# Kernel tuning notes

Hardware: AMD Instinct MI355X
Metric: run time of the kernel (lower is better)

Reference implementation:

```python
import jax, jax.numpy as jnp
import numpy as np

INP = 512
HIDDEN = 512
N_HEADS = 8          # called 'head_dim' in the torch code
D_HEAD = HIDDEN // N_HEADS  # 64
BASE = 10000.0
SCALE = D_HEAD ** (-0.5)


def rope(x):
    # x: [b, s, h, d]
    b, s, h, d = x.shape
    half = d // 2
    theta = 1.0 / (BASE ** (jnp.arange(0, d, 2, dtype=jnp.float32) / d))  # [d/2]
    idx_theta = jnp.arange(s, dtype=jnp.float32)[:, None] * theta[None, :]  # [s, d/2]
    idx_theta2 = jnp.concatenate([idx_theta, idx_theta], axis=1)            # [s, d]
    neg_half = jnp.concatenate([-x[..., half:], x[..., :half]], axis=-1)
    cos = jnp.cos(idx_theta2)[None, :, None, :]
    sin = jnp.sin(idx_theta2)[None, :, None, :]
    return x * cos + neg_half * sin


def setup_inputs() -> dict:
    key = jax.random.key(0)
    ks = jax.random.split(key, 10)
    b, s = 4, 2048
    init = lambda k, shp, fan_in: jax.random.normal(k, shp, jnp.float32) * (fan_in ** -0.5)
    return {
        "x": jax.random.normal(ks[0], (b, s, INP), jnp.float32),
        "c": jax.random.normal(ks[1], (b, s, INP), jnp.float32),
        "Wq": init(ks[2], (INP, HIDDEN), INP), "bq": jnp.zeros((HIDDEN,), jnp.float32),
        "Wk": init(ks[3], (INP, HIDDEN), INP), "bk": jnp.zeros((HIDDEN,), jnp.float32),
        "Wv": init(ks[4], (INP, HIDDEN), INP), "bv": jnp.zeros((HIDDEN,), jnp.float32),
        "Wo": init(ks[5], (HIDDEN, INP), HIDDEN), "bo": jnp.zeros((INP,), jnp.float32),
    }


def reference(x, c, Wq, bq, Wk, bk, Wv, bv, Wo, bo):
    b, s, _ = x.shape
    h_res = x
    q = (c @ Wq + bq).reshape(b, s, N_HEADS, D_HEAD)
    k = (x @ Wk + bk).reshape(b, s, N_HEADS, D_HEAD)
    v = (x @ Wv + bv).reshape(b, s, N_HEADS, D_HEAD)
    q = rope(q)
    k = rope(k)  # computed but unused, exactly as in the source
    # NOTE: source computes scores between q and V (not k) -- faithful reproduction
    att = jnp.einsum('bihd,bjhd->bhij', q, v)            # [b, h, s, s]
    att = jax.nn.softmax(att * SCALE, axis=-1)
    out = jnp.einsum('bhij,bjhd->bihd', att, v)          # [b, s, h, d]
    out = out.reshape(b, s, HIDDEN)
    out = out @ Wo + bo
    return out + h_res
```

## Files before the change

kernel.cpp:

```cpp
#include <hip/hip_runtime.h>
#include <hip/hip_bf16.h>
#include <cstdint>

typedef float f32x4 __attribute__((ext_vector_type(4)));
typedef short bf16x8 __attribute__((ext_vector_type(8)));
typedef short bf16x4 __attribute__((ext_vector_type(4)));
typedef unsigned short u16;

#define B_    4
#define S_    2048
#define H_    8
#define D_    64
#define M_    8192

#define OFF_CBF   0UL
#define OFF_XBF   8388608UL
#define OFF_QBH   16777216UL
#define OFF_VBH   25165824UL
#define OFF_VTBH  33554432UL
#define OFF_ATTN  41943040UL
#define OFF_WQT   50331648UL
#define OFF_WVT   50855936UL
#define OFF_WOT   51380224UL
#define OFF_BIAS  51904512UL
#define OFF_COS   51910656UL
#define OFF_SIN   52172800UL
#define WS_NEEDED 52434944UL

__device__ __forceinline__ u16 f2bf(float f){
    union { float f; uint32_t u; } v; v.f = f;
    uint32_t r = (v.u + 0x7fffu + ((v.u >> 16) & 1u)) >> 16;
    return (u16)r;
}
__device__ __forceinline__ float bf2f(u16 h){
    union { uint32_t u; float f; } v; v.u = ((uint32_t)h) << 16;
    return v.f;
}
__device__ __forceinline__ uint32_t fbits(float f){
    union { float f; uint32_t u; } v; v.f = f; return v.u;
}

__device__ __forceinline__ f32x4 mfma16(bf16x4 a, bf16x4 b, f32x4 c){
#if __has_builtin(__builtin_amdgcn_mfma_f32_16x16x16bf16_1k)
    return __builtin_amdgcn_mfma_f32_16x16x16bf16_1k(a, b, c, 0, 0, 0);
#else
    asm volatile("v_mfma_f32_16x16x16_bf16 %0, %1, %2, %0" : "+v"(c) : "v"(a), "v"(b));
    return c;
#endif
}

__device__ __forceinline__ int swz(int row, int col){
    return (col & ~63) | ((((col >> 3) & 7) ^ (row & 7)) << 3) | (col & 7);
}

__device__ __forceinline__ int detect_f32(const void* x_in){
    int lane = threadIdx.x & 63;
    ushort2 dv = ((const ushort2*)x_in)[lane];
    bool hit = ((((dv.x >> 7) & 0xFF) >= 160) || (((dv.y >> 7) & 0xFF) >= 160));
    return __ballot(hit) != 0ULL;
}

__device__ __forceinline__ void gload_lds16(const u16* g, u16* l){
    __builtin_amdgcn_global_load_lds(
        (const __attribute__((address_space(1))) void*)g,
        (__attribute__((address_space(3))) void*)l, 16, 0, 0);
}

__global__ void k_prep(const void* c_in, const void* x_in,
                       const void* Wq, const void* Wv, const void* Wo,
                       const void* bq, const void* bv, const void* bo,
                       u16* c_bf, u16* x_bf,
                       u16* Wqt, u16* Wvt, u16* Wot, float* bias_ws,
                       float* cos_t, float* sin_t){
    int bid = blockIdx.x;
    if (bid >= 11264){
        int idx = (bid - 11264) * 256 + threadIdx.x;
        int pos = idx >> 5, j = idx & 31;
        double theta = pow(10000.0, -(double)j / 32.0);
        double rev = ((double)pos * theta) * 0.15915494309189535;
        rev -= floor(rev);
        float fr = (float)rev;
        cos_t[idx] = __builtin_amdgcn_cosf(fr);
        sin_t[idx] = __builtin_amdgcn_sinf(fr);
        return;
    }
    if (bid >= 8192){
        int f = detect_f32(x_in);
        int wi = (bid - 8192) >> 10;
        int idx = ((bid - 8192) & 1023) * 256 + threadIdx.x;
        int k = idx >> 9, n = idx & 511;
        const void* W; u16* Wt; const void* bb;
        if (wi == 0){ W = Wq; Wt = Wqt; bb = bq; }
        else if (wi == 1){ W = Wv; Wt = Wvt; bb = bv; }
        else { W = Wo; Wt = Wot; bb = bo; }
        float v = f ? ((const float*)W)[idx] : bf2f(((const u16*)W)[idx]);
        Wt[n * 512 + swz(n, k)] = f2bf(v);
        if (idx < 512){
            float b = f ? ((const float*)bb)[idx] : bf2f(((const u16*)bb)[idx]);
            bias_ws[wi * 512 + idx] = b;
        }
        return;
    }
    int f = detect_f32(x_in);
    int isx = bid >= 4096;
    int t = (bid & 4095) * 256 + threadIdx.x;
    const void* src = isx ? x_in : c_in;
    u16* dst = isx ? x_bf : c_bf;
    int e0 = t * 4, row = e0 >> 9, col = e0 & 511;
    size_t didx = (size_t)row * 512 + swz(row, col);
    ushort4 o;
    if (f){
        float4 v = ((const float4*)src)[t];
        o.x = f2bf(v.x); o.y = f2bf(v.y); o.z = f2bf(v.z); o.w = f2bf(v.w);
    } else {
        o = ((const ushort4*)src)[t];
    }
    *(ushort4*)(dst + didx) = o;
}

__global__ __launch_bounds__(256) void k_gemm_qv(
    const u16* __restrict__ c_bf, const u16* __restrict__ x_bf,
    const u16* __restrict__ Wqt, const u16* __restrict__ Wvt,
    const float* __restrict__ bias_ws,
    const float* __restrict__ cos_t, const float* __restrict__ sin_t,
    u16* __restrict__ Qbh, u16* __restrict__ Vbh, u16* __restrict__ Vtbh)
{
    __shared__ __align__(16) u16 Als[2][128 * 64];
    __shared__ __align__(16) u16 Bls[2][128 * 64];
    const int w = threadIdx.x >> 6, lane = threadIdx.x & 63;
    const int g = lane >> 4, cq = lane & 15;
    const int wm = w & 1, wn = w >> 1;
    const int z = blockIdx.z;
    const u16* A  = z ? x_bf : c_bf;
    const u16* Wt = z ? Wvt : Wqt;
    const float* bias = bias_ws + (z ? 512 : 0);
    const int m0b = blockIdx.x * 128, n0b = blockIdx.y * 128;
    const int m0 = m0b + wm * 64, n0 = n0b + wn * 64;
    const int swzi = ((cq & 7) << 3);

    int srow[4], scol[4];
    #pragma unroll
    for (int i = 0; i < 4; i++){
        int flat = (w * 4 + i) * 64 + lane;
        srow[i] = flat >> 3; scol[i] = (flat & 7) * 8;
    }

    const f32x4 zero = {0.f, 0.f, 0.f, 0.f};
    f32x4 acc[4][4];
    #pragma unroll
    for (int i = 0; i < 4; i++)
        #pragma unroll
        for (int j = 0; j < 4; j++) acc[i][j] = zero;

    #pragma unroll
    for (int i = 0; i < 4; i++){
        gload_lds16(A  + (size_t)(m0b + srow[i]) * 512 + scol[i], &Als[0][(w*4 + i) * 512]);
        gload_lds16(Wt + (size_t)(n0b + srow[i]) * 512 + scol[i], &Bls[0][(w*4 + i) * 512]);
    }

    for (int kt = 0; kt < 8; kt++){
        const int buf = kt & 1;
        __builtin_amdgcn_s_waitcnt(0x0F70);
        __syncthreads();
        if (kt < 7){
            const int kk = (kt + 1) * 64;
            #pragma unroll
            for (int i = 0; i < 4; i++){
                gload_lds16(A  + (size_t)(m0b + srow[i]) * 512 + kk + scol[i], &Als[buf^1][(w*4 + i) * 512]);
                gload_lds16(Wt + (size_t)(n0b + srow[i]) * 512 + kk + scol[i], &Bls[buf^1][(w*4 + i) * 512]);
            }
        }
        #pragma unroll
        for (int ks = 0; ks < 2; ks++){
            const int cs = ((ks * 4 + g) << 3) ^ swzi;
            bf16x8 a[4], b[4];
            #pragma unroll
            for (int mt = 0; mt < 4; mt++)
                a[mt] = *(const bf16x8*)&Als[buf][(wm*64 + mt*16 + cq) * 64 + cs];
            #pragma unroll
            for (int nt = 0; nt < 4; nt++)
                b[nt] = *(const bf16x8*)&Bls[buf][(wn*64 + nt*16 + cq) * 64 + cs];
            #pragma unroll
            for (int mt = 0; mt < 4; mt++)
                #pragma unroll
                for (int nt = 0; nt < 4; nt++)
                    acc[mt][nt] = __builtin_amdgcn_mfma_f32_16x16x32_bf16(a[mt], b[nt], acc[mt][nt], 0, 0, 0);
        }
    }
    __syncthreads();

    #pragma unroll
    for (int nt = 0; nt < 4; nt++){
        float bvv = bias[n0 + nt*16 + cq];
        #pragma unroll
        for (int mt = 0; mt < 4; mt++) acc[mt][nt] += bvv;
    }
    const int h = n0 >> 6;
    if (z == 0){
        const float SCL = 0.125f * 1.4426950408889634f;
        #pragma unroll
        for (int mt = 0; mt < 4; mt++){
            #pragma unroll
            for (int r = 0; r < 4; r++){
                int row = m0 + mt*16 + g*4 + r;
                int b_idx = row >> 11, si = row & 2047;
                size_t base = ((size_t)(b_idx*8 + h) * 2048 + si) * 64;
                #pragma unroll
                for (int nt = 0; nt < 2; nt++){
                    int dj = nt*16 + cq;
                    float cv = cos_t[si*32 + dj], sv = sin_t[si*32 + dj];
                    float x1 = acc[mt][nt][r], x2 = acc[mt][nt+2][r];
                    Qbh[base + dj]      = f2bf((x1*cv - x2*sv) * SCL);
                    Qbh[base + dj + 32] = f2bf((x2*cv + x1*sv) * SCL);
                }
            }
        }
    } else {
        float* ltw = ((float*)&Als[0][0]) + w * (16 * 65);
        const int b_idx = m0 >> 11, si0 = m0 & 2047;
        const size_t tbase = ((size_t)(b_idx*8 + h) * 64) * 2048;
        #pragma unroll
        for (int mt = 0; mt < 4; mt++)
            #pragma unroll
            for (int r = 0; r < 4; r++){
                int row = m0 + mt*16 + g*4 + r;
                int bi = row >> 11, si = row & 2047;
                size_t base = ((size_t)(bi*8 + h) * 2048 + si) * 64;
                int s7 = si & 7;
                #pragma unroll
                for (int nt = 0; nt < 4; nt++){
                    int dj = nt*16 + cq;
                    int col = ((((dj >> 3) ^ s7) & 7) << 3) | (dj & 7);
                    Vbh[base + col] = f2bf(acc[mt][nt][r]);
                }
            }
        #pragma unroll
        for (int nt = 0; nt < 4; nt++){
            #pragma unroll
            for (int mt = 0; mt < 4; mt++)
                #pragma unroll
                for (int r = 0; r < 4; r++)
                    ltw[cq * 65 + mt*16 + g*4 + r] = acc[mt][nt][r];
            __builtin_amdgcn_wave_barrier();
            #pragma unroll
            for (int dd = 0; dd < 16; dd++){
                float v = ltw[dd * 65 + lane];
                int col = ((((lane >> 3) ^ (dd & 7)) & 7) << 3) | (lane & 7);
                Vtbh[tbase + (size_t)(nt*16 + dd) * 2048 + si0 + col] = f2bf(v);
            }
            __builtin_amdgcn_wave_barrier();
        }
    }
}

__global__ __launch_bounds__(256) void k_attn(
    const u16* __restrict__ Qbh, const u16* __restrict__ Vbh,
    const u16* __restrict__ Vtbh, u16* __restrict__ attn)
{
    __shared__ __align__(16) u16 Vs[2][64 * 64];
    __shared__ __align__(16) u16 Vts[2][64 * 64];
    const int w = threadIdx.x >> 6, lane = threadIdx.x & 63;
    const int g = lane >> 4, cq = lane & 15;
    const int s7 = cq & 7;
    const int bh = blockIdx.y;
    const int i0 = blockIdx.x * 128 + w * 32;

    bf16x8 aq[2][2];
    #pragma unroll
    for (int mt = 0; mt < 2; mt++)
        #pragma unroll
        for (int kk = 0; kk < 2; kk++)
            aq[mt][kk] = *(const bf16x8*)(Qbh + ((size_t)bh*2048 + i0 + mt*16 + cq)*64 + kk*32 + g*8);

    const int c0 = (w * 2) * 512, c1 = c0 + 512;
    const u16* gvs0 = Vbh + (size_t)bh * 131072 + c0 + lane * 8;
    const u16* gvs1 = gvs0 + 512;
    const int dr0 = (w * 2) * 8 + (lane >> 3);
    const u16* gvt0 = Vtbh + ((size_t)bh * 64 + dr0) * 2048 + (lane & 7) * 8;
    const u16* gvt1 = gvt0 + 8 * 2048;

    gload_lds16(gvs0, &Vs[0][c0]);
    gload_lds16(gvs1, &Vs[0][c1]);
    gload_lds16(gvt0, &Vts[0][c0]);
    gload_lds16(gvt1, &Vts[0][c1]);

    const f32x4 zero = {0.f, 0.f, 0.f, 0.f};
    f32x4 o[2][4]; float fl[2] = {0.f, 0.f};
    #pragma unroll
    for (int mt = 0; mt < 2; mt++)
        #pragma unroll
        for (int t = 0; t < 4; t++) o[mt][t] = zero;

    for (int jt = 0; jt < 32; jt++){
        const int buf = jt & 1;
        __builtin_amdgcn_s_waitcnt(0x0F70);
        __syncthreads();
        if (jt < 31){
            const size_t os = (size_t)(jt + 1) * 4096, ot = (size_t)(jt + 1) * 64;
            gload_lds16(gvs0 + os, &Vs[buf^1][c0]);
            gload_lds16(gvs1 + os, &Vs[buf^1][c1]);
            gload_lds16(gvt0 + ot, &Vts[buf^1][c0]);
            gload_lds16(gvt1 + ot, &Vts[buf^1][c1]);
        }
        bf16x4 pk[2][4];
        #pragma unroll
        for (int t = 0; t < 4; t++){
            bf16x8 bv0 = *(const bf16x8*)&Vs[buf][(t*16 + cq)*64 + ((g ^ s7) << 3)];
            bf16x8 bv1 = *(const bf16x8*)&Vs[buf][(t*16 + cq)*64 + (((4 + g) ^ s7) << 3)];
            #pragma unroll
            for (int mt = 0; mt < 2; mt++){
                f32x4 s = __builtin_amdgcn_mfma_f32_16x16x32_bf16(bv0, aq[mt][0], zero, 0, 0, 0);
                s = __builtin_amdgcn_mfma_f32_16x16x32_bf16(bv1, aq[mt][1], s, 0, 0, 0);
                #pragma unroll
                for (int r = 0; r < 4; r++) s[r] = __builtin_amdgcn_exp2f(s[r]);
                fl[mt] += (s[0] + s[1]) + (s[2] + s[3]);
                union { bf16x4 v; uint32_t wd[2]; } u;
                u.wd[0] = (fbits(s[0]) >> 16) | (fbits(s[1]) & 0xffff0000u);
                u.wd[1] = (fbits(s[2]) >> 16) | (fbits(s[3]) & 0xffff0000u);
                pk[mt][t] = u.v;
            }
        }
        #pragma unroll
        for (int t = 0; t < 4; t++){
            const int chk = ((t*2 + (g >> 1)) ^ s7) & 7;
            #pragma unroll
            for (int tn = 0; tn < 4; tn++){
                bf16x4 bt = *(const bf16x4*)&Vts[buf][(tn*16 + cq)*64 + (chk << 3) + (g & 1)*4];
                o[0][tn] = mfma16(bt, pk[0][t], o[0][tn]);
                o[1][tn] = mfma16(bt, pk[1][t], o[1][tn]);
            }
        }
    }
    const int b_idx = bh >> 3, h = bh & 7;
    #pragma unroll
    for (int mt = 0; mt < 2; mt++){
        float sum = fl[mt];
        sum += __shfl_xor(sum, 16);
        sum += __shfl_xor(sum, 32);
        float inv = 1.f / sum;
        int row = b_idx*2048 + i0 + mt*16 + cq;
        #pragma unroll
        for (int tn = 0; tn < 4; tn++){
            f32x4 ov = o[mt][tn] * inv;
            uint2 pw;
            pw.x = (fbits(ov[0]) >> 16) | (fbits(ov[1]) & 0xffff0000u);
            pw.y = (fbits(ov[2]) >> 16) | (fbits(ov[3]) & 0xffff0000u);
            int chunk = ((tn*2 + (g >> 1)) ^ s7) & 7;
            int col = h*64 + (chunk << 3) + (g & 1)*4;
            *(uint2*)&attn[(size_t)row * 512 + col] = pw;
        }
    }
}

__global__ __launch_bounds__(256) void k_gemm_out(
    const u16* __restrict__ attn, const u16* __restrict__ Wot,
    const float* __restrict__ bias_ws, const void* __restrict__ x_in,
    void* __restrict__ out)
{
    __shared__ __align__(16) u16 Als[2][128 * 64];
    __shared__ __align__(16) u16 Bls[2][64 * 64];
    const int w = threadIdx.x >> 6, lane = threadIdx.x & 63;
    const int g = lane >> 4, cq = lane & 15;
    const int wm = w & 1, wn = w >> 1;
    const int m0b = blockIdx.x * 128, n0b = blockIdx.y * 64;
    const int m0 = m0b + wm * 64, n0 = n0b + wn * 32;
    const int f = detect_f32(x_in);
    const int swzi = ((cq & 7) << 3);

    int sra[4], sca[4], srb[2], scb[2];
    #pragma unroll
    for (int i = 0; i < 4; i++){
        int flat = (w * 4 + i) * 64 + lane;
        sra[i] = flat >> 3; sca[i] = (flat & 7) * 8;
    }
    #pragma unroll
    for (int i = 0; i < 2; i++){
        int flat = (w * 2 + i) * 64 + lane;
        srb[i] = flat >> 3; scb[i] = (flat & 7) * 8;
    }

    const f32x4 zero = {0.f, 0.f, 0.f, 0.f};
    f32x4 acc[4][2];
    #pragma unroll
    for (int i = 0; i < 4; i++)
        #pragma unroll
        for (int j = 0; j < 2; j++) acc[i][j] = zero;

    #pragma unroll
    for (int i = 0; i < 4; i++)
        gload_lds16(attn + (size_t)(m0b + sra[i]) * 512 + sca[i], &Als[0][(w*4 + i) * 512]);
    #pragma unroll
    for (int i = 0; i < 2; i++)
        gload_lds16(Wot + (size_t)(n0b + srb[i]) * 512 + scb[i], &Bls[0][(w*2 + i) * 512]);

    for (int kt = 0; kt < 8; kt++){
        const int buf = kt & 1;
        __builtin_amdgcn_s_waitcnt(0x0F70);
        __syncthreads();
        if (kt < 7){
            const int kk = (kt + 1) * 64;
            #pragma unroll
            for (int i = 0; i < 4; i++)
                gload_lds16(attn + (size_t)(m0b + sra[i]) * 512 + kk + sca[i], &Als[buf^1][(w*4 + i) * 512]);
            #pragma unroll
            for (int i = 0; i < 2; i++)
                gload_lds16(Wot + (size_t)(n0b + srb[i]) * 512 + kk + scb[i], &Bls[buf^1][(w*2 + i) * 512]);
        }
        #pragma unroll
        for (int ks = 0; ks < 2; ks++){
            const int cs = ((ks * 4 + g) << 3) ^ swzi;
            bf16x8 a[4], b[2];
            #pragma unroll
            for (int mt = 0; mt < 4; mt++)
                a[mt] = *(const bf16x8*)&Als[buf][(wm*64 + mt*16 + cq) * 64 + cs];
            #pragma unroll
            for (int nt = 0; nt < 2; nt++)
                b[nt] = *(const bf16x8*)&Bls[buf][(wn*32 + nt*16 + cq) * 64 + cs];
            #pragma unroll
            for (int mt = 0; mt < 4; mt++)
                #pragma unroll
                for (int nt = 0; nt < 2; nt++)
                    acc[mt][nt] = __builtin_amdgcn_mfma_f32_16x16x32_bf16(a[mt], b[nt], acc[mt][nt], 0, 0, 0);
        }
    }
    #pragma unroll
    for (int mt = 0; mt < 4; mt++)
        #pragma unroll
        for (int nt = 0; nt < 2; nt++)
            #pragma unroll
            for (int r = 0; r < 4; r++){
                int row = m0 + mt*16 + g*4 + r;
                int col = n0 + nt*16 + cq;
                size_t idx = (size_t)row * 512 + col;
                float resid = f ? ((const float*)x_in)[idx] : bf2f(((const u16*)x_in)[idx]);
                float v = acc[mt][nt][r] + bias_ws[1024 + col] + resid;
                if (f) ((float*)out)[idx] = v;
                else   ((u16*)out)[idx] = f2bf(v);
            }
}

extern "C" void kernel_launch(void* const* d_in, const int* in_sizes, int n_in,
                              void* d_out, int out_size, void* d_ws, size_t ws_size,
                              hipStream_t stream){
    const void* x_in = d_in[0];
    const void* c_in = d_in[1];
    const void* Wq = d_in[2]; const void* bq = d_in[3];
    const void* Wv = d_in[6]; const void* bv = d_in[7];
    const void* Wo = d_in[8]; const void* bo = d_in[9];

    if (ws_size < WS_NEEDED){
        hipMemsetAsync(d_out, 0, (size_t)out_size * 2, stream);
        return;
    }
    char* ws = (char*)d_ws;
    u16* c_bf  = (u16*)(ws + OFF_CBF);
    u16* x_bf  = (u16*)(ws + OFF_XBF);
    u16* Qbh   = (u16*)(ws + OFF_QBH);
    u16* Vbh   = (u16*)(ws + OFF_VBH);
    u16* Vtbh  = (u16*)(ws + OFF_VTBH);
    u16* attn  = (u16*)(ws + OFF_ATTN);
    u16* Wqt   = (u16*)(ws + OFF_WQT);
    u16* Wvt   = (u16*)(ws + OFF_WVT);
    u16* Wot   = (u16*)(ws + OFF_WOT);
    float* bias_ws = (float*)(ws + OFF_BIAS);
    float* cos_t   = (float*)(ws + OFF_COS);
    float* sin_t   = (float*)(ws + OFF_SIN);

    k_prep<<<11520, 256, 0, stream>>>(c_in, x_in, Wq, Wv, Wo, bq, bv, bo,
                                      c_bf, x_bf, Wqt, Wvt, Wot, bias_ws, cos_t, sin_t);
    k_gemm_qv<<<dim3(64, 4, 2), 256, 0, stream>>>(c_bf, x_bf, Wqt, Wvt, bias_ws,
                                                  cos_t, sin_t, Qbh, Vbh, Vtbh);
    k_attn<<<dim3(16, 32), 256, 0, stream>>>(Qbh, Vbh, Vtbh, attn);
    k_gemm_out<<<dim3(64, 8), 256, 0, stream>>>(attn, Wot, bias_ws, x_in, d_out);
}
```

Measured before the change: 196.4 us.

## Split attention over key halves and merge partial sums in output GEMM

The attention kernel now splits the key/value sequence into two halves along a new grid z dimension. Each half writes unnormalized bf16 partial outputs and row sums, which the output projection GEMM combines and normalizes while staging its A tile. The change also replaces the XOR-swizzled LDS layouts and direct global-to-LDS loads with padded (stride 68) rows loaded through registers, and adds an occupancy hint. The aim is to double the attention block count for better CU utilization. In exchange it adds an extra partial-buffer round trip, conversion work in the GEMM prologue, and a second bf16 rounding of the partials.

```diff
diff --git a/kernel.cpp b/kernel.cpp
--- a/kernel.cpp
+++ b/kernel.cpp
@@ -94,7 +94,7 @@
         else if (wi == 1){ W = Wv; Wt = Wvt; bb = bv; }
         else { W = Wo; Wt = Wot; bb = bo; }
         float v = f ? ((const float*)W)[idx] : bf2f(((const u16*)W)[idx]);
-        Wt[n * 512 + swz(n, k)] = f2bf(v);
+        Wt[n * 512 + (wi == 2 ? k : swz(n, k))] = f2bf(v);
         if (idx < 512){
             float b = f ? ((const float*)bb)[idx] : bf2f(((const u16*)bb)[idx]);
             bias_ws[wi * 512 + idx] = b;
@@ -226,13 +226,9 @@
                 int row = m0 + mt*16 + g*4 + r;
                 int bi = row >> 11, si = row & 2047;
                 size_t base = ((size_t)(bi*8 + h) * 2048 + si) * 64;
-                int s7 = si & 7;
-                #pragma unroll
-                for (int nt = 0; nt < 4; nt++){
-                    int dj = nt*16 + cq;
-                    int col = ((((dj >> 3) ^ s7) & 7) << 3) | (dj & 7);
-                    Vbh[base + col] = f2bf(acc[mt][nt][r]);
-                }
+                #pragma unroll
+                for (int nt = 0; nt < 4; nt++)
+                    Vbh[base + nt*16 + cq] = f2bf(acc[mt][nt][r]);
             }
         #pragma unroll
         for (int nt = 0; nt < 4; nt++){
@@ -245,25 +241,25 @@
             #pragma unroll
             for (int dd = 0; dd < 16; dd++){
                 float v = ltw[dd * 65 + lane];
-                int col = ((((lane >> 3) ^ (dd & 7)) & 7) << 3) | (lane & 7);
-                Vtbh[tbase + (size_t)(nt*16 + dd) * 2048 + si0 + col] = f2bf(v);
+                Vtbh[tbase + (size_t)(nt*16 + dd) * 2048 + si0 + lane] = f2bf(v);
             }
             __builtin_amdgcn_wave_barrier();
         }
     }
 }
 
-__global__ __launch_bounds__(256) void k_attn(
+__global__ __launch_bounds__(256, 4) void k_attn(
     const u16* __restrict__ Qbh, const u16* __restrict__ Vbh,
-    const u16* __restrict__ Vtbh, u16* __restrict__ attn)
+    const u16* __restrict__ Vtbh,
+    u16* __restrict__ part0, u16* __restrict__ part1, float* __restrict__ lsum)
 {
-    __shared__ __align__(16) u16 Vs[2][64 * 64];
-    __shared__ __align__(16) u16 Vts[2][64 * 64];
+    __shared__ __align__(16) u16 Vs[2][64 * 68];
+    __shared__ __align__(16) u16 Vts[2][64 * 68];
     const int w = threadIdx.x >> 6, lane = threadIdx.x & 63;
     const int g = lane >> 4, cq = lane & 15;
-    const int s7 = cq & 7;
-    const int bh = blockIdx.y;
+    const int bh = blockIdx.y, z = blockIdx.z;
     const int i0 = blockIdx.x * 128 + w * 32;
+    const int j0 = z * 1024;
 
     bf16x8 aq[2][2];
     #pragma unroll
@@ -272,17 +268,17 @@
         for (int kk = 0; kk < 2; kk++)
             aq[mt][kk] = *(const bf16x8*)(Qbh + ((size_t)bh*2048 + i0 + mt*16 + cq)*64 + kk*32 + g*8);
 
-    const int c0 = (w * 2) * 512, c1 = c0 + 512;
-    const u16* gvs0 = Vbh + (size_t)bh * 131072 + c0 + lane * 8;
-    const u16* gvs1 = gvs0 + 512;
-    const int dr0 = (w * 2) * 8 + (lane >> 3);
-    const u16* gvt0 = Vtbh + ((size_t)bh * 64 + dr0) * 2048 + (lane & 7) * 8;
-    const u16* gvt1 = gvt0 + 8 * 2048;
-
-    gload_lds16(gvs0, &Vs[0][c0]);
-    gload_lds16(gvs1, &Vs[0][c1]);
-    gload_lds16(gvt0, &Vts[0][c0]);
-    gload_lds16(gvt1, &Vts[0][c1]);
+    const int sr = w * 16 + (lane >> 2), sc = (lane & 3) * 16;
+    const u16* gvs = Vbh  + ((size_t)bh*2048 + j0 + sr) * 64 + sc;
+    const u16* gvt = Vtbh + ((size_t)bh*64 + sr) * 2048 + j0 + sc;
+    const int ls = sr * 68 + sc;
+
+    {
+        bf16x8 a0 = *(const bf16x8*)gvs,       a1 = *(const bf16x8*)(gvs + 8);
+        bf16x8 b0 = *(const bf16x8*)gvt,       b1 = *(const bf16x8*)(gvt + 8);
+        *(bf16x8*)&Vs[0][ls]  = a0;  *(bf16x8*)&Vs[0][ls + 8]  = a1;
+        *(bf16x8*)&Vts[0][ls] = b0;  *(bf16x8*)&Vts[0][ls + 8] = b1;
+    }
 
     const f32x4 zero = {0.f, 0.f, 0.f, 0.f};
     f32x4 o[2][4]; float fl[2] = {0.f, 0.f};
@@ -291,22 +287,21 @@
         #pragma unroll
         for (int t = 0; t < 4; t++) o[mt][t] = zero;
 
-    for (int jt = 0; jt < 32; jt++){
+    for (int jt = 0; jt < 16; jt++){
         const int buf = jt & 1;
-        __builtin_amdgcn_s_waitcnt(0x0F70);
         __syncthreads();
-        if (jt < 31){
-            const size_t os = (size_t)(jt + 1) * 4096, ot = (size_t)(jt + 1) * 64;
-            gload_lds16(gvs0 + os, &Vs[buf^1][c0]);
-            gload_lds16(gvs1 + os, &Vs[buf^1][c1]);
-            gload_lds16(gvt0 + ot, &Vts[buf^1][c0]);
-            gload_lds16(gvt1 + ot, &Vts[buf^1][c1]);
+        bf16x8 na0, na1, nb0, nb1;
+        if (jt < 15){
+            na0 = *(const bf16x8*)(gvs + (size_t)(jt + 1) * 4096);
+            na1 = *(const bf16x8*)(gvs + (size_t)(jt + 1) * 4096 + 8);
+            nb0 = *(const bf16x8*)(gvt + (size_t)(jt + 1) * 64);
+            nb1 = *(const bf16x8*)(gvt + (size_t)(jt + 1) * 64 + 8);
         }
         bf16x4 pk[2][4];
         #pragma unroll
         for (int t = 0; t < 4; t++){
-            bf16x8 bv0 = *(const bf16x8*)&Vs[buf][(t*16 + cq)*64 + ((g ^ s7) << 3)];
-            bf16x8 bv1 = *(const bf16x8*)&Vs[buf][(t*16 + cq)*64 + (((4 + g) ^ s7) << 3)];
+            bf16x8 bv0 = *(const bf16x8*)&Vs[buf][(t*16 + cq)*68 + g*8];
+            bf16x8 bv1 = *(const bf16x8*)&Vs[buf][(t*16 + cq)*68 + 32 + g*8];
             #pragma unroll
             for (int mt = 0; mt < 2; mt++){
                 f32x4 s = __builtin_amdgcn_mfma_f32_16x16x32_bf16(bv0, aq[mt][0], zero, 0, 0, 0);
@@ -321,51 +316,54 @@
             }
         }
         #pragma unroll
-        for (int t = 0; t < 4; t++){
-            const int chk = ((t*2 + (g >> 1)) ^ s7) & 7;
+        for (int t = 0; t < 4; t++)
             #pragma unroll
             for (int tn = 0; tn < 4; tn++){
-                bf16x4 bt = *(const bf16x4*)&Vts[buf][(tn*16 + cq)*64 + (chk << 3) + (g & 1)*4];
+                bf16x4 bt = *(const bf16x4*)&Vts[buf][(tn*16 + cq)*68 + t*16 + g*4];
                 o[0][tn] = mfma16(bt, pk[0][t], o[0][tn]);
                 o[1][tn] = mfma16(bt, pk[1][t], o[1][tn]);
             }
+        if (jt < 15){
+            *(bf16x8*)&Vs[buf^1][ls]  = na0;  *(bf16x8*)&Vs[buf^1][ls + 8]  = na1;
+            *(bf16x8*)&Vts[buf^1][ls] = nb0;  *(bf16x8*)&Vts[buf^1][ls + 8] = nb1;
         }
     }
     const int b_idx = bh >> 3, h = bh & 7;
+    u16* part = z ? part1 : part0;
     #pragma unroll
     for (int mt = 0; mt < 2; mt++){
         float sum = fl[mt];
         sum += __shfl_xor(sum, 16);
         sum += __shfl_xor(sum, 32);
-        float inv = 1.f / sum;
         int row = b_idx*2048 + i0 + mt*16 + cq;
+        if (lane < 16)
+            lsum[(size_t)z*65536 + (size_t)h*8192 + row] = sum;
         #pragma unroll
         for (int tn = 0; tn < 4; tn++){
-            f32x4 ov = o[mt][tn] * inv;
+            f32x4 ov = o[mt][tn];
             uint2 pw;
-            pw.x = (fbits(ov[0]) >> 16) | (fbits(ov[1]) & 0xffff0000u);
-            pw.y = (fbits(ov[2]) >> 16) | (fbits(ov[3]) & 0xffff0000u);
-            int chunk = ((tn*2 + (g >> 1)) ^ s7) & 7;
-            int col = h*64 + (chunk << 3) + (g & 1)*4;
-            *(uint2*)&attn[(size_t)row * 512 + col] = pw;
+            pw.x = (uint32_t)f2bf(ov[0]) | ((uint32_t)f2bf(ov[1]) << 16);
+            pw.y = (uint32_t)f2bf(ov[2]) | ((uint32_t)f2bf(ov[3]) << 16);
+            int col = h*64 + tn*16 + g*4;
+            *(uint2*)&part[(size_t)row * 512 + col] = pw;
         }
     }
 }
 
 __global__ __launch_bounds__(256) void k_gemm_out(
-    const u16* __restrict__ attn, const u16* __restrict__ Wot,
-    const float* __restrict__ bias_ws, const void* __restrict__ x_in,
-    void* __restrict__ out)
+    const u16* __restrict__ part0, const u16* __restrict__ part1,
+    const float* __restrict__ lsum,
+    const u16* __restrict__ Wot, const float* __restrict__ bias_ws,
+    const void* __restrict__ x_in, void* __restrict__ out)
 {
-    __shared__ __align__(16) u16 Als[2][128 * 64];
-    __shared__ __align__(16) u16 Bls[2][64 * 64];
+    __shared__ __align__(16) u16 Als[2][128 * 68];
+    __shared__ __align__(16) u16 Bls[2][64 * 68];
     const int w = threadIdx.x >> 6, lane = threadIdx.x & 63;
     const int g = lane >> 4, cq = lane & 15;
     const int wm = w & 1, wn = w >> 1;
     const int m0b = blockIdx.x * 128, n0b = blockIdx.y * 64;
     const int m0 = m0b + wm * 64, n0 = n0b + wn * 32;
     const int f = detect_f32(x_in);
-    const int swzi = ((cq & 7) << 3);
 
     int sra[4], sca[4], srb[2], scb[2];
     #pragma unroll
@@ -386,41 +384,72 @@
         #pragma unroll
         for (int j = 0; j < 2; j++) acc[i][j] = zero;
 
-    #pragma unroll
-    for (int i = 0; i < 4; i++)
-        gload_lds16(attn + (size_t)(m0b + sra[i]) * 512 + sca[i], &Als[0][(w*4 + i) * 512]);
+    bf16x8 pa0[4], pa1[4], pb[2]; float pr[4];
+    #pragma unroll
+    for (int i = 0; i < 4; i++){
+        int row = m0b + sra[i];
+        pa0[i] = *(const bf16x8*)&part0[(size_t)row * 512 + sca[i]];
+        pa1[i] = *(const bf16x8*)&part1[(size_t)row * 512 + sca[i]];
+        pr[i] = 1.f / (lsum[row] + lsum[65536 + row]);
+    }
     #pragma unroll
     for (int i = 0; i < 2; i++)
-        gload_lds16(Wot + (size_t)(n0b + srb[i]) * 512 + scb[i], &Bls[0][(w*2 + i) * 512]);
+        pb[i] = *(const bf16x8*)&Wot[(size_t)(n0b + srb[i]) * 512 + scb[i]];
+    #pragma unroll
+    for (int i = 0; i < 4; i++){
+        union { bf16x8 v; u16 e[8]; } a8;
+        #pragma unroll
+        for (int e = 0; e < 8; e++)
+            a8.e[e] = f2bf((bf2f((u16)pa0[i][e]) + bf2f((u16)pa1[i][e])) * pr[i]);
+        *(bf16x8*)&Als[0][sra[i]*68 + sca[i]] = a8.v;
+    }
+    #pragma unroll
+    for (int i = 0; i < 2; i++)
+        *(bf16x8*)&Bls[0][srb[i]*68 + scb[i]] = pb[i];
 
     for (int kt = 0; kt < 8; kt++){
         const int buf = kt & 1;
-        __builtin_amdgcn_s_waitcnt(0x0F70);
         __syncthreads();
         if (kt < 7){
-            const int kk = (kt + 1) * 64;
-            #pragma unroll
-            for (int i = 0; i < 4; i++)
-                gload_lds16(attn + (size_t)(m0b + sra[i]) * 512 + kk + sca[i], &Als[buf^1][(w*4 + i) * 512]);
+            const int kk = (kt + 1) * 64, h = kt + 1;
+            #pragma unroll
+            for (int i = 0; i < 4; i++){
+                int row = m0b + sra[i];
+                pa0[i] = *(const bf16x8*)&part0[(size_t)row * 512 + kk + sca[i]];
+                pa1[i] = *(const bf16x8*)&part1[(size_t)row * 512 + kk + sca[i]];
+                pr[i] = 1.f / (lsum[(size_t)h*8192 + row] + lsum[65536 + (size_t)h*8192 + row]);
+            }
             #pragma unroll
             for (int i = 0; i < 2; i++)
-                gload_lds16(Wot + (size_t)(n0b + srb[i]) * 512 + kk + scb[i], &Bls[buf^1][(w*2 + i) * 512]);
+                pb[i] = *(const bf16x8*)&Wot[(size_t)(n0b + srb[i]) * 512 + kk + scb[i]];
         }
         #pragma unroll
         for (int ks = 0; ks < 2; ks++){
-            const int cs = ((ks * 4 + g) << 3) ^ swzi;
             bf16x8 a[4], b[2];
             #pragma unroll
             for (int mt = 0; mt < 4; mt++)
-                a[mt] = *(const bf16x8*)&Als[buf][(wm*64 + mt*16 + cq) * 64 + cs];
+                a[mt] = *(const bf16x8*)&Als[buf][(wm*64 + mt*16 + cq)*68 + ks*32 + g*8];
             #pragma unroll
             for (int nt = 0; nt < 2; nt++)
-                b[nt] = *(const bf16x8*)&Bls[buf][(wn*32 + nt*16 + cq) * 64 + cs];
+                b[nt] = *(const bf16x8*)&Bls[buf][(wn*32 + nt*16 + cq)*68 + ks*32 + g*8];
             #pragma unroll
             for (int mt = 0; mt < 4; mt++)
                 #pragma unroll
                 for (int nt = 0; nt < 2; nt++)
                     acc[mt][nt] = __builtin_amdgcn_mfma_f32_16x16x32_bf16(a[mt], b[nt], acc[mt][nt], 0, 0, 0);
+        }
+        if (kt < 7){
+            #pragma unroll
+            for (int i = 0; i < 4; i++){
+                union { bf16x8 v; u16 e[8]; } a8;
+                #pragma unroll
+                for (int e = 0; e < 8; e++)
+                    a8.e[e] = f2bf((bf2f((u16)pa0[i][e]) + bf2f((u16)pa1[i][e])) * pr[i]);
+                *(bf16x8*)&Als[buf^1][sra[i]*68 + sca[i]] = a8.v;
+            }
+            #pragma unroll
+            for (int i = 0; i < 2; i++)
+                *(bf16x8*)&Bls[buf^1][srb[i]*68 + scb[i]] = pb[i];
         }
     }
     #pragma unroll
@@ -458,7 +487,9 @@
     u16* Qbh   = (u16*)(ws + OFF_QBH);
     u16* Vbh   = (u16*)(ws + OFF_VBH);
     u16* Vtbh  = (u16*)(ws + OFF_VTBH);
-    u16* attn  = (u16*)(ws + OFF_ATTN);
+    u16* part0 = (u16*)(ws + OFF_ATTN);
+    u16* part1 = (u16*)(ws + OFF_CBF);
+    float* lsum = (float*)(ws + OFF_XBF);
     u16* Wqt   = (u16*)(ws + OFF_WQT);
     u16* Wvt   = (u16*)(ws + OFF_WVT);
     u16* Wot   = (u16*)(ws + OFF_WOT);
@@ -470,6 +501,7 @@
                                       c_bf, x_bf, Wqt, Wvt, Wot, bias_ws, cos_t, sin_t);
     k_gemm_qv<<<dim3(64, 4, 2), 256, 0, stream>>>(c_bf, x_bf, Wqt, Wvt, bias_ws,
                                                   cos_t, sin_t, Qbh, Vbh, Vtbh);
-    k_attn<<<dim3(16, 32), 256, 0, stream>>>(Qbh, Vbh, Vtbh, attn);
-    k_gemm_out<<<dim3(64, 8), 256, 0, stream>>>(attn, Wot, bias_ws, x_in, d_out);
-}
+    k_attn<<<dim3(16, 32, 2), 256, 0, stream>>>(Qbh, Vbh, Vtbh, part0, part1, lsum);
+    k_gemm_out<<<dim3(64, 8), 256, 0, stream>>>(part0, part1, lsum, Wot, bias_ws,
+                                                x_in, d_out);
+}
```

New measurement: 191.7 us. 1.02x faster.
